# Performance work log

Hardware: AMD Instinct MI355X
Metric: run time of the kernel (lower is better)

## Reference

```python
import jax, jax.numpy as jnp
import numpy as np

# Module config (matches init_kwargs)
H, W = 512, 512          # in_dims
KH, KW = 32, 32          # kernel_dims
SH, SW = 16, 16          # stride
PH, PW = 8, 8            # padding
B = 64                   # batch
FULL_H, FULL_W = H + 2 * PH, W + 2 * PW            # 528, 528
NKH = 1 + (FULL_H - KH) // SH                      # 32
NKW = 1 + (FULL_W - KW) // SW                      # 32
NK = NKH * NKW                                     # 1024 output positions


def _patch_indices() -> np.ndarray:
    """Flat indices into the padded image for each sliding window.

    Reproduces the connectivity matrix columns of _create_connectivity_matrix:
    window k starts at (row*SH)*FULL_W + col*SW. Returns (NK, KH*KW) int32.
    """
    dr, dc = np.meshgrid(np.arange(KH), np.arange(KW), indexing="ij")
    off = (dr * FULL_W + dc).reshape(-1)                       # (KH*KW,)
    starts = (np.arange(NKH)[:, None] * SH * FULL_W
              + np.arange(NKW)[None, :] * SW).reshape(-1)      # (NK,)
    return (starts[:, None] + off[None, :]).astype(np.int32)


_IDX = jnp.asarray(_patch_indices())  # (NK, KH*KW), constant layout


def setup_inputs() -> dict:
    key = jax.random.key(0)
    kx, kw, kb = jax.random.split(key, 3)
    x = jax.random.normal(kx, (B, 1, H, W), dtype=jnp.float32)
    # Per-window weights = BSR values of the masked dense (padded_total, NK) matrix.
    # Xavier-normal scale of the underlying dense linear.
    std = float(np.sqrt(2.0 / (FULL_H * FULL_W + NK)))
    weight = jax.random.normal(kw, (NK, KH * KW), dtype=jnp.float32) * std
    bias = jax.random.normal(kb, (NK,), dtype=jnp.float32) * 0.01
    return {"x": x, "weight": weight, "bias": bias}


def reference(x, weight, bias):
    # x: (B, 1, H, W) -> pad -> flatten to (B, FULL_H*FULL_W)
    xp = jnp.pad(x, ((0, 0), (0, 0), (PH, PH), (PW, PW)))
    xf = xp.reshape(x.shape[0], FULL_H * FULL_W)
    # Gather the KHxKW window for every output position: (B, NK, KH*KW).
    patches = jnp.take(xf, _IDX, axis=1)
    # Untied locally-connected contraction (the block-sparse GEMM) + bias.
    out = jnp.einsum("bnk,nk->bn", patches, weight) + bias
    return out.reshape(x.shape[0], NKH, NKW)
```

## Files before the change

### kernel.cpp

```cpp
#include <hip/hip_runtime.h>

#define IMG_H 512
#define IMG_W 512
#define IMG_SZ (IMG_H * IMG_W)
#define NKH 32
#define NKW 32
#define NK 1024
#define BATCH 64
#define NTT 33
#define NTILE (NTT * NTT)
#define BG 4
#define NBLK (NTILE * BG)

typedef __attribute__((address_space(3))) char lds_char_t;
typedef const __attribute__((address_space(1))) char g_char_t;

__global__ __launch_bounds__(256)
void bslc_init(const float* __restrict__ bias, float* __restrict__ out)
{
    const int g = blockIdx.x * 256 + threadIdx.x;
    out[g] = bias[g & (NK - 1)];
}

__global__ __launch_bounds__(256, 8)
void bslc_main(const float* __restrict__ x,
               const float* __restrict__ w,
               float* __restrict__ out)
{
    __shared__ float4 xs[16 * 64];
    __shared__ float4 wl[4 * 64];

    const int hw = blockIdx.x;
    const int xcd = hw & 7, sl = hw >> 3;
    const int q8 = NBLK >> 3, r8 = NBLK & 7;
    const int work = (xcd < r8 ? xcd * (q8 + 1)
                               : r8 * (q8 + 1) + (xcd - r8) * q8) + sl;

    const int bg  = work & 3;
    const int lin = work >> 2;
    const int tr = lin / NTT, tc = lin % NTT;

    const int t = threadIdx.x, lane = t & 63, wv = t >> 6;

    const int qr = wv >> 1, qc = wv & 1;
    const int nr = tr - qr, nc = tc - qc;
    const bool valid = (nr >= 0) & (nr < NKH) & (nc >= 0) & (nc < NKW);
    const int n = nr * NKW + nc;

    if (valid) {
        const int kq = lane;
        const size_t off = (size_t)n * 1024
                         + (size_t)(qr * 16 + (kq >> 2)) * 32
                         + qc * 16 + (kq & 3) * 4;
        wl[wv * 64 + kq] = *reinterpret_cast<const float4*>(w + off);
    }

    const int r0 = tr * 16 - 8, c0 = tc * 16 - 8;
    const bool interior = (tr >= 1) & (tr <= 31) & (tc >= 1) & (tc <= 31);

    if (interior) {
#pragma unroll
        for (int ii = 0; ii < 4; ++ii) {
            const int bl = 4 * ii + wv;
            const int c  = lane ^ bl;
            const float* gp = x + (size_t)(bg * 16 + bl) * IMG_SZ
                            + (size_t)(r0 + (c >> 2)) * IMG_W
                            + c0 + (c & 3) * 4;
            __builtin_amdgcn_global_load_lds(
                (g_char_t*)gp, (lds_char_t*)&xs[bl * 64], 16, 0, 0);
        }
    } else {
#pragma unroll
        for (int ii = 0; ii < 4; ++ii) {
            const int bl = 4 * ii + wv;
            const int c  = lane ^ bl;
            const int rimg = r0 + (c >> 2);
            const int cimg = c0 + (c & 3) * 4;
            float4 v = make_float4(0.f, 0.f, 0.f, 0.f);
            if (rimg >= 0 && rimg < IMG_H && cimg >= 0 && cimg < IMG_W)
                v = *reinterpret_cast<const float4*>(
                    x + (size_t)(bg * 16 + bl) * IMG_SZ
                      + (size_t)rimg * IMG_W + cimg);
            xs[bl * 64 + lane] = v;
        }
    }
    __syncthreads();

    if (!valid) return;

    const int p  = lane >> 4;
    const int bl = lane & 15;

    float a0 = 0.f, a1 = 0.f, a2 = 0.f, a3 = 0.f;
#pragma unroll
    for (int j = 0; j < 16; ++j) {
        const int kq = 4 * j + p;
        const float4 xv  = xs[bl * 64 + (kq ^ bl)];
        const float4 wv4 = wl[wv * 64 + kq];
        a0 = fmaf(xv.x, wv4.x, a0);
        a1 = fmaf(xv.y, wv4.y, a1);
        a2 = fmaf(xv.z, wv4.z, a2);
        a3 = fmaf(xv.w, wv4.w, a3);
    }
    float s = (a0 + a1) + (a2 + a3);
    s += __shfl_xor(s, 16, 64);
    s += __shfl_xor(s, 32, 64);
    if (p == 0)
        atomicAdd(&out[(size_t)(bg * 16 + bl) * NK + n], s);
}

extern "C" void kernel_launch(void* const* d_in, const int* in_sizes, int n_in,
                              void* d_out, int out_size, void* d_ws, size_t ws_size,
                              hipStream_t stream) {
    const float* x    = (const float*)d_in[0];
    const float* wgt  = (const float*)d_in[1];
    const float* bias = (const float*)d_in[2];
    float* out        = (float*)d_out;

    bslc_init<<<dim3(BATCH * NK / 256), 256, 0, stream>>>(bias, out);
    bslc_main<<<dim3(NBLK), 256, 0, stream>>>(x, wgt, out);
}
```

Measured before the change: 107.6 us.

## Loop batch groups inside each block with double-buffered LDS staging

Each block now handles all four 16-image batch groups of a tile instead of launching one block per group. The next group's image tile is staged into a second LDS buffer while the current group is computed, and the weight tile is loaded once per block through a direct global-to-LDS load. This is meant to amortise the weight load and hide global latency behind compute. In exchange the grid is four times smaller, LDS use per block doubles, the occupancy hint is lowered, and each group iteration adds a block-wide barrier.

```diff
diff --git a/kernel.cpp b/kernel.cpp
--- a/kernel.cpp
+++ b/kernel.cpp
@@ -6,11 +6,8 @@
 #define NKH 32
 #define NKW 32
 #define NK 1024
-#define BATCH 64
 #define NTT 33
 #define NTILE (NTT * NTT)
-#define BG 4
-#define NBLK (NTILE * BG)
 
 typedef __attribute__((address_space(3))) char lds_char_t;
 typedef const __attribute__((address_space(1))) char g_char_t;
@@ -22,23 +19,20 @@
     out[g] = bias[g & (NK - 1)];
 }
 
-__global__ __launch_bounds__(256, 8)
+__global__ __launch_bounds__(256, 4)
 void bslc_main(const float* __restrict__ x,
                const float* __restrict__ w,
                float* __restrict__ out)
 {
-    __shared__ float4 xs[16 * 64];
+    __shared__ float4 xs[2][16 * 64];
     __shared__ float4 wl[4 * 64];
 
     const int hw = blockIdx.x;
     const int xcd = hw & 7, sl = hw >> 3;
-    const int q8 = NBLK >> 3, r8 = NBLK & 7;
+    const int q8 = NTILE >> 3, r8 = NTILE & 7;
     const int work = (xcd < r8 ? xcd * (q8 + 1)
                                : r8 * (q8 + 1) + (xcd - r8) * q8) + sl;
-
-    const int bg  = work & 3;
-    const int lin = work >> 2;
-    const int tr = lin / NTT, tc = lin % NTT;
+    const int tr = work / NTT, tc = work % NTT;
 
     const int t = threadIdx.x, lane = t & 63, wv = t >> 6;
 
@@ -48,17 +42,20 @@
     const int n = nr * NKW + nc;
 
     if (valid) {
-        const int kq = lane;
-        const size_t off = (size_t)n * 1024
-                         + (size_t)(qr * 16 + (kq >> 2)) * 32
-                         + qc * 16 + (kq & 3) * 4;
-        wl[wv * 64 + kq] = *reinterpret_cast<const float4*>(w + off);
+        const float* gw = w + (size_t)n * 1024
+                        + (size_t)(qr * 16 + (lane >> 2)) * 32
+                        + qc * 16 + (lane & 3) * 4;
+        __builtin_amdgcn_global_load_lds(
+            (g_char_t*)gw, (lds_char_t*)&wl[wv * 64], 16, 0, 0);
+    } else {
+        wl[wv * 64 + lane] = make_float4(0.f, 0.f, 0.f, 0.f);
     }
 
     const int r0 = tr * 16 - 8, c0 = tc * 16 - 8;
     const bool interior = (tr >= 1) & (tr <= 31) & (tc >= 1) & (tc <= 31);
+    const int p = lane >> 4, bl16 = lane & 15;
 
-    if (interior) {
+    auto stage_dma = [&](int bg, int buf) {
 #pragma unroll
         for (int ii = 0; ii < 4; ++ii) {
             const int bl = 4 * ii + wv;
@@ -67,9 +64,10 @@
                             + (size_t)(r0 + (c >> 2)) * IMG_W
                             + c0 + (c & 3) * 4;
             __builtin_amdgcn_global_load_lds(
-                (g_char_t*)gp, (lds_char_t*)&xs[bl * 64], 16, 0, 0);
+                (g_char_t*)gp, (lds_char_t*)&xs[buf][bl * 64], 16, 0, 0);
         }
-    } else {
+    };
+    auto border_load = [&](int bg, float4* brd) {
 #pragma unroll
         for (int ii = 0; ii < 4; ++ii) {
             const int bl = 4 * ii + wv;
@@ -81,32 +79,56 @@
                 v = *reinterpret_cast<const float4*>(
                     x + (size_t)(bg * 16 + bl) * IMG_SZ
                       + (size_t)rimg * IMG_W + cimg);
-            xs[bl * 64 + lane] = v;
+            brd[ii] = v;
         }
+    };
+    auto border_write = [&](int buf, const float4* brd) {
+#pragma unroll
+        for (int ii = 0; ii < 4; ++ii) {
+            const int bl = 4 * ii + wv;
+            xs[buf][bl * 64 + lane] = brd[ii];
+        }
+    };
+
+    float4 brd[4];
+    if (interior) {
+        stage_dma(0, 0);
+    } else {
+        border_load(0, brd);
+        border_write(0, brd);
     }
     __syncthreads();
 
-    if (!valid) return;
+#pragma unroll
+    for (int bg = 0; bg < 4; ++bg) {
+        const int cur = bg & 1, nxt = cur ^ 1;
 
-    const int p  = lane >> 4;
-    const int bl = lane & 15;
+        if (bg < 3) {
+            if (interior) stage_dma(bg + 1, nxt);
+            else          border_load(bg + 1, brd);
+        }
 
-    float a0 = 0.f, a1 = 0.f, a2 = 0.f, a3 = 0.f;
+        float a0 = 0.f, a1 = 0.f, a2 = 0.f, a3 = 0.f;
 #pragma unroll
-    for (int j = 0; j < 16; ++j) {
-        const int kq = 4 * j + p;
-        const float4 xv  = xs[bl * 64 + (kq ^ bl)];
-        const float4 wv4 = wl[wv * 64 + kq];
-        a0 = fmaf(xv.x, wv4.x, a0);
-        a1 = fmaf(xv.y, wv4.y, a1);
-        a2 = fmaf(xv.z, wv4.z, a2);
-        a3 = fmaf(xv.w, wv4.w, a3);
+        for (int j = 0; j < 16; ++j) {
+            const int kq = 4 * j + p;
+            const float4 xv  = xs[cur][bl16 * 64 + (kq ^ bl16)];
+            const float4 wv4 = wl[wv * 64 + kq];
+            a0 = fmaf(xv.x, wv4.x, a0);
+            a1 = fmaf(xv.y, wv4.y, a1);
+            a2 = fmaf(xv.z, wv4.z, a2);
+            a3 = fmaf(xv.w, wv4.w, a3);
+        }
+        float s = (a0 + a1) + (a2 + a3);
+        s += __shfl_xor(s, 16, 64);
+        s += __shfl_xor(s, 32, 64);
+        if (valid && p == 0)
+            atomicAdd(&out[(size_t)(bg * 16 + bl16) * NK + n], s);
+
+        if (bg < 3 && !interior) border_write(nxt, brd);
+
+        __syncthreads();
     }
-    float s = (a0 + a1) + (a2 + a3);
-    s += __shfl_xor(s, 16, 64);
-    s += __shfl_xor(s, 32, 64);
-    if (p == 0)
-        atomicAdd(&out[(size_t)(bg * 16 + bl) * NK + n], s);
 }
 
 extern "C" void kernel_launch(void* const* d_in, const int* in_sizes, int n_in,
@@ -117,6 +139,6 @@
     const float* bias = (const float*)d_in[2];
     float* out        = (float*)d_out;
 
-    bslc_init<<<dim3(BATCH * NK / 256), 256, 0, stream>>>(bias, out);
-    bslc_main<<<dim3(NBLK), 256, 0, stream>>>(x, wgt, out);
+    bslc_init<<<dim3(64 * NK / 256), 256, 0, stream>>>(bias, out);
+    bslc_main<<<dim3(NTILE), 256, 0, stream>>>(x, wgt, out);
 }
```

Measured after the change: 109.1 us. About the same (+1.4%).
